# Kernel tuning notes

Measured on AMD Instinct MI355X. Metric: run time of the kernel, lower is better.

## Reference

```python
import jax, jax.numpy as jnp
import numpy as np

TOP_K = 8
ROUTED_SCALING_FACTOR = 1.0
EPS = 1e-20


def setup_inputs() -> dict:
    key = jax.random.key(0)
    k1, k2, k3 = jax.random.split(key, 3)
    T, D, E = 8192, 4096, 64
    x = jax.random.normal(k1, (T, D), dtype=jnp.float32)
    gate_weight = jax.random.normal(k2, (E, D), dtype=jnp.float32) * (1.0 / np.sqrt(D))
    bias = jax.random.normal(k3, (E,), dtype=jnp.float32) * 0.1
    return {"x": x, "gate_weight": gate_weight, "bias": bias}


def reference(x, gate_weight, bias):
    # logits: [T, E] = x [T, D] @ gate_weight.T [D, E]
    logits = jnp.einsum('td,ed->te', x.astype(jnp.float32), gate_weight)
    scores = jax.nn.sigmoid(logits)
    biased = scores + bias  # broadcast [E]
    # top-k on biased scores, sorted descending
    _, indices = jax.lax.top_k(biased, TOP_K)  # [T, K]
    selected_scores = jnp.take_along_axis(scores, indices, axis=-1)  # [T, K]
    normalized = selected_scores / (jnp.sum(selected_scores, axis=-1, keepdims=True) + EPS)
    weights = normalized * ROUTED_SCALING_FACTOR
    return (indices, weights)
```

## Files before the change

### kernel.cpp

```cpp
#include <hip/hip_runtime.h>
#include <math.h>

#define T_TOK 8192
#define DDIM  4096
#define NEXP  64
#define TOPK  8
#define WAVES 8
#define STEPS 16

typedef __attribute__((ext_vector_type(8))) _Float16 half8;
typedef __attribute__((ext_vector_type(4))) float f32x4;

#define RS 2048.0f

__global__ __launch_bounds__(256) void pack_w(
    const float* __restrict__ gw, _Float16* __restrict__ wpk)
{
    const int g    = blockIdx.x * 256 + threadIdx.x;
    const int lane = g & 63;
    const int n    = (g >> 6) & 3;
    const int kt   = g >> 8;
    const int e    = n * 16 + (lane & 15);
    const int k    = kt * 32 + (lane >> 4) * 8;

    const float* src = gw + (size_t)e * DDIM + k;
    float4 v0 = *reinterpret_cast<const float4*>(src);
    float4 v1 = *reinterpret_cast<const float4*>(src + 4);
    const float v[8] = {v0.x, v0.y, v0.z, v0.w, v1.x, v1.y, v1.z, v1.w};

    half8 h0, h1;
    #pragma unroll
    for (int j = 0; j < 8; j++) {
        _Float16 a = (_Float16)v[j];
        h0[j] = a;
        h1[j] = (_Float16)((v[j] - (float)a) * RS);
    }
    size_t base = ((size_t)(kt * 4 + n) * 2) * 512;
    *reinterpret_cast<half8*>(wpk + base + lane * 8)       = h0;
    *reinterpret_cast<half8*>(wpk + base + 512 + lane * 8) = h1;
}

__global__ __launch_bounds__(512, 2) void gemm_topk(
    const float* __restrict__ x, const _Float16* __restrict__ wpk,
    const float* __restrict__ bias, float* __restrict__ out)
{
    __shared__ float red[WAVES][32][NEXP];

    const int tid  = threadIdx.x;
    const int lane = tid & 63;
    const int wv   = tid >> 6;
    const int tok0 = blockIdx.x * 32;
    const int am   = lane & 15;
    const int ag   = lane >> 4;

    const float* xr0 = x + (size_t)(tok0 + am) * DDIM + wv * (DDIM / WAVES) + ag * 8;
    const float* xr1 = xr0 + (size_t)16 * DDIM;
    const _Float16* bbase = wpk + (size_t)(wv * STEPS) * 8 * 512 + lane * 8;

    f32x4 aH[2][4], aM[2][4];
    #pragma unroll
    for (int t = 0; t < 2; t++)
        #pragma unroll
        for (int n = 0; n < 4; n++) {
            aH[t][n] = (f32x4){0.f, 0.f, 0.f, 0.f};
            aM[t][n] = (f32x4){0.f, 0.f, 0.f, 0.f};
        }

    float4 av[3][4];
    half8  bf[2][8];

    #pragma unroll
    for (int st = 0; st < 2; st++) {
        av[st][0] = *reinterpret_cast<const float4*>(xr0 + st * 32);
        av[st][1] = *reinterpret_cast<const float4*>(xr0 + st * 32 + 4);
        av[st][2] = *reinterpret_cast<const float4*>(xr1 + st * 32);
        av[st][3] = *reinterpret_cast<const float4*>(xr1 + st * 32 + 4);
    }
    #pragma unroll
    for (int n = 0; n < 4; n++) {
        bf[0][2 * n]     = *reinterpret_cast<const half8*>(bbase + n * 1024);
        bf[0][2 * n + 1] = *reinterpret_cast<const half8*>(bbase + n * 1024 + 512);
    }

    #pragma unroll
    for (int st = 0; st < STEPS; st++) {
        const int cur  = st & 1;
        const int nxt  = cur ^ 1;
        const int acur = st % 3;

        if (st + 2 < STEPS) {
            const int ap = (st + 2) % 3;
            av[ap][0] = *reinterpret_cast<const float4*>(xr0 + (st + 2) * 32);
            av[ap][1] = *reinterpret_cast<const float4*>(xr0 + (st + 2) * 32 + 4);
            av[ap][2] = *reinterpret_cast<const float4*>(xr1 + (st + 2) * 32);
            av[ap][3] = *reinterpret_cast<const float4*>(xr1 + (st + 2) * 32 + 4);
        }
        if (st + 1 < STEPS) {
            const _Float16* bp = bbase + (size_t)(st + 1) * 8 * 512;
            #pragma unroll
            for (int n = 0; n < 4; n++) {
                bf[nxt][2 * n]     = *reinterpret_cast<const half8*>(bp + n * 1024);
                bf[nxt][2 * n + 1] = *reinterpret_cast<const half8*>(bp + n * 1024 + 512);
            }
        }

        half8 a0[2], a1[2];
        #pragma unroll
        for (int t = 0; t < 2; t++) {
            const float* vv = reinterpret_cast<const float*>(&av[acur][2 * t]);
            #pragma unroll
            for (int j = 0; j < 8; j++) {
                float v = vv[j];
                _Float16 h = (_Float16)v;
                a0[t][j] = h;
                a1[t][j] = (_Float16)((v - (float)h) * RS);
            }
        }
        #pragma unroll
        for (int t = 0; t < 2; t++)
            #pragma unroll
            for (int n = 0; n < 4; n++) {
                aH[t][n] = __builtin_amdgcn_mfma_f32_16x16x32_f16(a0[t], bf[cur][2 * n],     aH[t][n], 0, 0, 0);
                aM[t][n] = __builtin_amdgcn_mfma_f32_16x16x32_f16(a0[t], bf[cur][2 * n + 1], aM[t][n], 0, 0, 0);
                aM[t][n] = __builtin_amdgcn_mfma_f32_16x16x32_f16(a1[t], bf[cur][2 * n],     aM[t][n], 0, 0, 0);
            }
    }

    const float i1 = 1.0f / RS;
    #pragma unroll
    for (int t = 0; t < 2; t++)
        #pragma unroll
        for (int n = 0; n < 4; n++)
            #pragma unroll
            for (int r = 0; r < 4; r++)
                red[wv][t * 16 + ag * 4 + r][n * 16 + am]
                    = aH[t][n][r] + aM[t][n][r] * i1;
    __syncthreads();

    {
        const int tok = tid >> 4;
        const int c4  = tid & 15;
        float4 s0 = *reinterpret_cast<const float4*>(&red[0][tok][c4 * 4]);
        #pragma unroll
        for (int s = 1; s < WAVES; s++) {
            float4 v = *reinterpret_cast<const float4*>(&red[s][tok][c4 * 4]);
            s0.x += v.x; s0.y += v.y; s0.z += v.z; s0.w += v.w;
        }
        *reinterpret_cast<float4*>(&red[0][tok][c4 * 4]) = s0;
    }
    __syncthreads();

    const float bsv = bias[lane];
    #pragma unroll
    for (int ti = 0; ti < 4; ti++) {
        const int tk = wv * 4 + ti;
        float logit  = red[0][tk][lane];
        float score  = 1.f / (1.f + expf(-logit));
        float biased = score + bsv;
        float my_sc = 0.f; int my_idx = 0; float ssum = 0.f;
        #pragma unroll
        for (int j = 0; j < TOPK; j++) {
            float vb = biased; int ib = lane;
            #pragma unroll
            for (int off = 32; off >= 1; off >>= 1) {
                float ov = __shfl_xor(vb, off);
                int   oi = __shfl_xor(ib, off);
                if (ov > vb || (ov == vb && oi < ib)) { vb = ov; ib = oi; }
            }
            float s_sel = __shfl(score, ib);
            ssum += s_sel;
            if (lane == j) { my_idx = ib; my_sc = s_sel; }
            if (lane == ib) biased = -INFINITY;
        }
        if (lane < TOPK) {
            out[(size_t)(tok0 + tk) * TOPK + lane] = (float)my_idx;
            out[(size_t)T_TOK * TOPK + (size_t)(tok0 + tk) * TOPK + lane]
                = my_sc / (ssum + 1e-20f);
        }
    }
}

extern "C" void kernel_launch(void* const* d_in, const int* in_sizes, int n_in,
                              void* d_out, int out_size, void* d_ws, size_t ws_size,
                              hipStream_t stream) {
    (void)in_sizes; (void)n_in; (void)out_size; (void)ws_size;
    const float* x    = (const float*)d_in[0];
    const float* gw   = (const float*)d_in[1];
    const float* bias = (const float*)d_in[2];
    float* out = (float*)d_out;
    _Float16* wpk = (_Float16*)d_ws;

    pack_w<<<128, 256, 0, stream>>>(gw, wpk);
    gemm_topk<<<T_TOK / 32, 512, 0, stream>>>(x, wpk, bias, out);
}
```

Measured before the change: 54.56 us.

## Stream x tiles via global_load_lds ring buffer with 16-token blocks

Replaces register-staged x loads with direct global-to-LDS async loads into a per-wave triple-buffered ring, paced by explicit vmcnt waits. Halves the tokens per block to 16 so twice as many blocks launch, and raises the occupancy hint to 4 blocks per CU. The weight fragments are now loaded each step without double buffering. The aim is to cut register pressure and raise occupancy to hide HBM latency, at the cost of doubling weight-fragment traffic per token and relying on hand-tuned waitcnt counts.

```diff
diff --git a/kernel.cpp b/kernel.cpp
--- a/kernel.cpp
+++ b/kernel.cpp
@@ -1,5 +1,6 @@
 #include <hip/hip_runtime.h>
 #include <math.h>
+#include <stdint.h>
 
 #define T_TOK 8192
 #define DDIM  4096
@@ -7,11 +8,12 @@
 #define TOPK  8
 #define WAVES 8
 #define STEPS 16
+#define RS    2048.0f
 
 typedef __attribute__((ext_vector_type(8))) _Float16 half8;
 typedef __attribute__((ext_vector_type(4))) float f32x4;
-
-#define RS 2048.0f
+typedef __attribute__((address_space(3))) uint32_t lds_u32;
+typedef const __attribute__((address_space(1))) uint32_t glb_u32;
 
 __global__ __launch_bounds__(256) void pack_w(
     const float* __restrict__ gw, _Float16* __restrict__ wpk)
@@ -40,121 +42,123 @@
     *reinterpret_cast<half8*>(wpk + base + 512 + lane * 8) = h1;
 }
 
-__global__ __launch_bounds__(512, 2) void gemm_topk(
+__global__ __launch_bounds__(512, 4) void gemm_topk(
     const float* __restrict__ x, const _Float16* __restrict__ wpk,
     const float* __restrict__ bias, float* __restrict__ out)
 {
-    __shared__ float red[WAVES][32][NEXP];
+    __shared__ float smem[WAVES * 3 * 512];
 
     const int tid  = threadIdx.x;
     const int lane = tid & 63;
     const int wv   = tid >> 6;
-    const int tok0 = blockIdx.x * 32;
+    const int tok0 = blockIdx.x * 16;
     const int am   = lane & 15;
     const int ag   = lane >> 4;
 
-    const float* xr0 = x + (size_t)(tok0 + am) * DDIM + wv * (DDIM / WAVES) + ag * 8;
-    const float* xr1 = xr0 + (size_t)16 * DDIM;
+    float* ring = smem + wv * (3 * 512);
+    const float* xr = x + (size_t)(tok0 + am) * DDIM + wv * (DDIM / WAVES) + ag * 8;
     const _Float16* bbase = wpk + (size_t)(wv * STEPS) * 8 * 512 + lane * 8;
 
-    f32x4 aH[2][4], aM[2][4];
-    #pragma unroll
-    for (int t = 0; t < 2; t++)
-        #pragma unroll
-        for (int n = 0; n < 4; n++) {
-            aH[t][n] = (f32x4){0.f, 0.f, 0.f, 0.f};
-            aM[t][n] = (f32x4){0.f, 0.f, 0.f, 0.f};
-        }
-
-    float4 av[3][4];
-    half8  bf[2][8];
-
-    #pragma unroll
-    for (int st = 0; st < 2; st++) {
-        av[st][0] = *reinterpret_cast<const float4*>(xr0 + st * 32);
-        av[st][1] = *reinterpret_cast<const float4*>(xr0 + st * 32 + 4);
-        av[st][2] = *reinterpret_cast<const float4*>(xr1 + st * 32);
-        av[st][3] = *reinterpret_cast<const float4*>(xr1 + st * 32 + 4);
-    }
+    f32x4 aH[4], aM[4];
     #pragma unroll
     for (int n = 0; n < 4; n++) {
-        bf[0][2 * n]     = *reinterpret_cast<const half8*>(bbase + n * 1024);
-        bf[0][2 * n + 1] = *reinterpret_cast<const half8*>(bbase + n * 1024 + 512);
+        aH[n] = (f32x4){0.f, 0.f, 0.f, 0.f};
+        aM[n] = (f32x4){0.f, 0.f, 0.f, 0.f};
     }
+
+#define ISSUE_A(st_, slot_) do {                                              \
+        const float* _s = xr + (st_) * 32;                                    \
+        __builtin_amdgcn_global_load_lds((glb_u32*)_s,                        \
+            (lds_u32*)(ring + (slot_) * 512), 16, 0, 0);                      \
+        __builtin_amdgcn_global_load_lds((glb_u32*)(_s + 4),                  \
+            (lds_u32*)(ring + (slot_) * 512 + 256), 16, 0, 0);                \
+    } while (0)
+
+    ISSUE_A(0, 0);
+    ISSUE_A(1, 1);
 
     #pragma unroll
     for (int st = 0; st < STEPS; st++) {
-        const int cur  = st & 1;
-        const int nxt  = cur ^ 1;
-        const int acur = st % 3;
+        if (st == 0)      asm volatile("s_waitcnt vmcnt(2)"  ::: "memory");
+        else if (st < 15) asm volatile("s_waitcnt vmcnt(10)" ::: "memory");
+        else              asm volatile("s_waitcnt vmcnt(8)"  ::: "memory");
+        __builtin_amdgcn_sched_barrier(0);
 
-        if (st + 2 < STEPS) {
-            const int ap = (st + 2) % 3;
-            av[ap][0] = *reinterpret_cast<const float4*>(xr0 + (st + 2) * 32);
-            av[ap][1] = *reinterpret_cast<const float4*>(xr0 + (st + 2) * 32 + 4);
-            av[ap][2] = *reinterpret_cast<const float4*>(xr1 + (st + 2) * 32);
-            av[ap][3] = *reinterpret_cast<const float4*>(xr1 + (st + 2) * 32 + 4);
-        }
-        if (st + 1 < STEPS) {
-            const _Float16* bp = bbase + (size_t)(st + 1) * 8 * 512;
-            #pragma unroll
-            for (int n = 0; n < 4; n++) {
-                bf[nxt][2 * n]     = *reinterpret_cast<const half8*>(bp + n * 1024);
-                bf[nxt][2 * n + 1] = *reinterpret_cast<const half8*>(bp + n * 1024 + 512);
-            }
-        }
+        const float* slotp = ring + (st % 3) * 512;
+        float4 v0 = *reinterpret_cast<const float4*>(slotp + lane * 4);
+        float4 v1 = *reinterpret_cast<const float4*>(slotp + 256 + lane * 4);
 
-        half8 a0[2], a1[2];
-        #pragma unroll
-        for (int t = 0; t < 2; t++) {
-            const float* vv = reinterpret_cast<const float*>(&av[acur][2 * t]);
+        half8 a0, a1;
+        {
+            const float vv[8] = {v0.x, v0.y, v0.z, v0.w, v1.x, v1.y, v1.z, v1.w};
             #pragma unroll
             for (int j = 0; j < 8; j++) {
                 float v = vv[j];
                 _Float16 h = (_Float16)v;
-                a0[t][j] = h;
-                a1[t][j] = (_Float16)((v - (float)h) * RS);
+                a0[j] = h;
+                a1[j] = (_Float16)((v - (float)h) * RS);
             }
         }
+
+        const _Float16* bp = bbase + (size_t)st * 4096;
+        half8 B0[4], B1[4];
         #pragma unroll
-        for (int t = 0; t < 2; t++)
-            #pragma unroll
-            for (int n = 0; n < 4; n++) {
-                aH[t][n] = __builtin_amdgcn_mfma_f32_16x16x32_f16(a0[t], bf[cur][2 * n],     aH[t][n], 0, 0, 0);
-                aM[t][n] = __builtin_amdgcn_mfma_f32_16x16x32_f16(a0[t], bf[cur][2 * n + 1], aM[t][n], 0, 0, 0);
-                aM[t][n] = __builtin_amdgcn_mfma_f32_16x16x32_f16(a1[t], bf[cur][2 * n],     aM[t][n], 0, 0, 0);
-            }
+        for (int n = 0; n < 4; n++) {
+            B0[n] = *reinterpret_cast<const half8*>(bp + n * 1024);
+            B1[n] = *reinterpret_cast<const half8*>(bp + n * 1024 + 512);
+        }
+
+        asm volatile("" ::: "memory");
+
+        if (st + 2 < STEPS) {
+            const int stn = st + 2;
+            ISSUE_A(stn, stn % 3);
+        }
+
+        #pragma unroll
+        for (int n = 0; n < 4; n++) {
+            aH[n] = __builtin_amdgcn_mfma_f32_16x16x32_f16(a0, B0[n], aH[n], 0, 0, 0);
+            aM[n] = __builtin_amdgcn_mfma_f32_16x16x32_f16(a0, B1[n], aM[n], 0, 0, 0);
+            aM[n] = __builtin_amdgcn_mfma_f32_16x16x32_f16(a1, B0[n], aM[n], 0, 0, 0);
+        }
     }
+#undef ISSUE_A
 
-    const float i1 = 1.0f / RS;
-    #pragma unroll
-    for (int t = 0; t < 2; t++)
+    __syncthreads();
+
+    {
+        const float i1 = 1.0f / RS;
+        float* red = smem;
         #pragma unroll
         for (int n = 0; n < 4; n++)
             #pragma unroll
             for (int r = 0; r < 4; r++)
-                red[wv][t * 16 + ag * 4 + r][n * 16 + am]
-                    = aH[t][n][r] + aM[t][n][r] * i1;
+                red[(size_t)(wv * 16 + ag * 4 + r) * 64 + n * 16 + am]
+                    = aH[n][r] + aM[n][r] * i1;
+    }
     __syncthreads();
 
-    {
+    if (tid < 256) {
+        float* red = smem;
         const int tok = tid >> 4;
         const int c4  = tid & 15;
-        float4 s0 = *reinterpret_cast<const float4*>(&red[0][tok][c4 * 4]);
+        float4 s0 = *reinterpret_cast<const float4*>(red + (size_t)tok * 64 + c4 * 4);
         #pragma unroll
         for (int s = 1; s < WAVES; s++) {
-            float4 v = *reinterpret_cast<const float4*>(&red[s][tok][c4 * 4]);
+            float4 v = *reinterpret_cast<const float4*>(
+                red + (size_t)(s * 16 + tok) * 64 + c4 * 4);
             s0.x += v.x; s0.y += v.y; s0.z += v.z; s0.w += v.w;
         }
-        *reinterpret_cast<float4*>(&red[0][tok][c4 * 4]) = s0;
+        *reinterpret_cast<float4*>(red + (size_t)tok * 64 + c4 * 4) = s0;
     }
     __syncthreads();
 
     const float bsv = bias[lane];
+    const float* red = smem;
     #pragma unroll
-    for (int ti = 0; ti < 4; ti++) {
-        const int tk = wv * 4 + ti;
-        float logit  = red[0][tk][lane];
+    for (int ti = 0; ti < 2; ti++) {
+        const int tk = wv * 2 + ti;
+        float logit  = red[(size_t)tk * 64 + lane];
         float score  = 1.f / (1.f + expf(-logit));
         float biased = score + bsv;
         float my_sc = 0.f; int my_idx = 0; float ssum = 0.f;
@@ -191,5 +195,5 @@
     _Float16* wpk = (_Float16*)d_ws;
 
     pack_w<<<128, 256, 0, stream>>>(gw, wpk);
-    gemm_topk<<<T_TOK / 32, 512, 0, stream>>>(x, wpk, bias, out);
+    gemm_topk<<<T_TOK / 16, 512, 0, stream>>>(x, wpk, bias, out);
 }
```

Result: no change. 54.39 us (-0.3%).
